# Optimization experiments

Hardware: AMD Instinct MI355X
Metric: run time of the kernel (lower is better)

## Reference

```python
import jax, jax.numpy as jnp
import numpy as np

B, N, E, H, D, MS, FF = 4, 500, 128, 8, 16, 16, 512
SQRT_D = 4.0  # sqrt_qkv_dim
EPS = 1e-5


def setup_inputs() -> dict:
    key = jax.random.key(0)
    ks = jax.random.split(key, 26)
    u = lambda k, sh, s: jax.random.uniform(k, sh, jnp.float32, -s, s)
    inp = {
        "x_edges_values": jax.random.uniform(ks[0], (B, N, N), jnp.float32),
        "depot_node_demand": jax.random.uniform(ks[1], (B, N, 1), jnp.float32),
        "rand": jax.random.uniform(ks[2], (B, E), jnp.float32),
        # attention projections (no bias)
        "Wq": u(ks[3], (E, H * D), E ** -0.5),
        "Wk": u(ks[4], (E, H * D), E ** -0.5),
        "Wv": u(ks[5], (E, H * D), E ** -0.5),
        # mixed-score per-head MLP
        "mix1_w": u(ks[6], (H, 2, MS), 0.7071067811865476),
        "mix1_b": u(ks[7], (H, MS), 0.7071067811865476),
        "mix2_w": u(ks[8], (H, MS, 1), 0.25),
        "mix2_b": u(ks[9], (H, 1), 0.25),
        # multi_head_combine
        "Wo": u(ks[10], (H * D, E), (H * D) ** -0.5),
        "bo": u(ks[11], (E,), (H * D) ** -0.5),
        # feed-forward
        "W1": u(ks[12], (E, FF), E ** -0.5),
        "b1": u(ks[13], (FF,), E ** -0.5),
        "W2": u(ks[14], (FF, E), FF ** -0.5),
        "b2": u(ks[15], (E,), FF ** -0.5),
        # batch norms (affine)
        "bn1_g": jnp.ones((E,), jnp.float32),
        "bn1_b": jnp.zeros((E,), jnp.float32),
        "bn2_g": jnp.ones((E,), jnp.float32),
        "bn2_b": jnp.zeros((E,), jnp.float32),
        # demand / node embeddings
        "Wd": u(ks[16], (1, E), 1.0),
        "bd": u(ks[17], (E,), 1.0),
        "Wn": u(ks[18], (2 * E, E), (2 * E) ** -0.5),
        "bn_node": u(ks[19], (E,), (2 * E) ** -0.5),
    }
    return inp


def _batchnorm(x, g, b):
    # BatchNorm1d in training mode over flattened [B*N, E]
    x2 = x.reshape(-1, E)
    m = x2.mean(0)
    v = ((x2 - m) ** 2).mean(0)  # biased variance, as torch uses for normalization
    return (((x2 - m) / jnp.sqrt(v + EPS)) * g + b).reshape(x.shape)


def reference(x_edges_values, depot_node_demand, rand, Wq, Wk, Wv,
              mix1_w, mix1_b, mix2_w, mix2_b, Wo, bo, W1, b1, W2, b2,
              bn1_g, bn1_b, bn2_g, bn2_b, Wd, bd, Wn, bn_node):
    # seed embeddings: row_emb zeros, col_emb scattered one-hot from a random perm
    row_emb = jnp.zeros((B, N, E), jnp.float32)
    perm = jnp.argsort(rand, axis=1)                       # [B, E] (seed_cnt = E since N > E)
    idx = jnp.concatenate([perm, perm, perm, perm], 1)[:, :N]  # 3E <= N < 4E branch
    col_emb = jax.nn.one_hot(idx, E, dtype=jnp.float32)    # [B, N, E]

    heads = lambda x: x.reshape(B, N, H, D).transpose(0, 2, 1, 3)  # [B,H,N,D]
    q = heads(row_emb @ Wq)
    k = heads(col_emb @ Wk)
    v = heads(col_emb @ Wv)

    dot = jnp.einsum('bhnd,bhmd->bhnm', q, k) / SQRT_D        # [B,H,N,N]
    cost = jnp.broadcast_to(x_edges_values[:, None], (B, H, N, N))
    two = jnp.stack([dot, cost], axis=-1)                      # [B,H,N,N,2]
    ms1 = jax.nn.relu(jnp.einsum('bhnmt,hts->bhnms', two, mix1_w)
                      + mix1_b[None, :, None, None, :])        # [B,H,N,N,MS]
    ms2 = jnp.einsum('bhnms,hso->bhnmo', ms1, mix2_w)[..., 0] \
          + mix2_b[None, :, None, :]                           # [B,H,N,N]
    weights = jax.nn.softmax(ms2, axis=-1)
    out = jnp.einsum('bhnm,bhmd->bhnd', weights, v)
    out_concat = out.transpose(0, 2, 1, 3).reshape(B, N, H * D)

    multi_head_out = out_concat @ Wo + bo
    out1 = _batchnorm(row_emb + multi_head_out, bn1_g, bn1_b)
    ff = jax.nn.relu(out1 @ W1 + b1) @ W2 + b2
    out3 = _batchnorm(out1 + ff, bn2_g, bn2_b)

    demand_feature = depot_node_demand @ Wd + bd               # [B,N,E]
    node_feature = jnp.concatenate([out3, demand_feature], -1) @ Wn + bn_node
    return node_feature
```

## Files before the change

kernel.cpp:

```cpp
#include <hip/hip_runtime.h>
#include <hip/hip_bf16.h>


#define BN_EPS 1e-5f
#define WS_X1    256000
#define WS_X2    512000
#define WS_SUM1  768000
#define WS_SQ1   768128
#define WS_SUM2  768256
#define WS_SQ2   768384
#define WS_UV    768512
#define WS_C0V   768640
#define BN1P     770000
#define BN2P     900000

#define GB8_R2(WPTR, LDW, KIDX, ACT2D, ACC)                             \
  {                                                                     \
    float4 w[8];                                                        \
    _Pragma("unroll")                                                   \
    for (int u = 0; u < 8; ++u)                                         \
      w[u] = *(const float4*)((WPTR) + (size_t)((KIDX) + u) * (LDW));   \
    _Pragma("unroll")                                                   \
    for (int u = 0; u < 8; ++u) {                                       \
      _Pragma("unroll")                                                 \
      for (int r = 0; r < 2; ++r) {                                     \
        float a = ACT2D[r][u];                                          \
        ACC[r][0] = fmaf(a, w[u].x, ACC[r][0]);                         \
        ACC[r][1] = fmaf(a, w[u].y, ACC[r][1]);                         \
        ACC[r][2] = fmaf(a, w[u].z, ACC[r][2]);                         \
        ACC[r][3] = fmaf(a, w[u].w, ACC[r][3]);                         \
      }                                                                 \
    }                                                                   \
  }

#define LD_AV2(SRC_ROW0, SRC_ROW1, KIDX, ACT2D)                         \
  {                                                                     \
    float4 x0 = *(const float4*)&(SRC_ROW0)[(KIDX)];                    \
    float4 y0 = *(const float4*)&(SRC_ROW0)[(KIDX) + 4];                \
    float4 x1 = *(const float4*)&(SRC_ROW1)[(KIDX)];                    \
    float4 y1 = *(const float4*)&(SRC_ROW1)[(KIDX) + 4];                \
    ACT2D[0][0]=x0.x; ACT2D[0][1]=x0.y; ACT2D[0][2]=x0.z; ACT2D[0][3]=x0.w; \
    ACT2D[0][4]=y0.x; ACT2D[0][5]=y0.y; ACT2D[0][6]=y0.z; ACT2D[0][7]=y0.w; \
    ACT2D[1][0]=x1.x; ACT2D[1][1]=x1.y; ACT2D[1][2]=x1.z; ACT2D[1][3]=x1.w; \
    ACT2D[1][4]=y1.x; ACT2D[1][5]=y1.y; ACT2D[1][6]=y1.z; ACT2D[1][7]=y1.w; \
  }

#define GB4_R4(WPTR, LDW, K0, SRC2D, ACC)                               \
  {                                                                     \
    float4 w[4];                                                        \
    _Pragma("unroll")                                                   \
    for (int u = 0; u < 4; ++u)                                         \
      w[u] = *(const float4*)((WPTR) + (size_t)((K0) + u) * (LDW));     \
    float av[4][4];                                                     \
    _Pragma("unroll")                                                   \
    for (int r = 0; r < 4; ++r) {                                       \
      float4 x = *(const float4*)&SRC2D[r][(K0)];                       \
      av[r][0] = x.x; av[r][1] = x.y; av[r][2] = x.z; av[r][3] = x.w;   \
    }                                                                   \
    _Pragma("unroll")                                                   \
    for (int u = 0; u < 4; ++u) {                                       \
      _Pragma("unroll")                                                 \
      for (int r = 0; r < 4; ++r) {                                     \
        ACC[r][0] = fmaf(av[r][u], w[u].x, ACC[r][0]);                  \
        ACC[r][1] = fmaf(av[r][u], w[u].y, ACC[r][1]);                  \
        ACC[r][2] = fmaf(av[r][u], w[u].z, ACC[r][2]);                  \
        ACC[r][3] = fmaf(av[r][u], w[u].w, ACC[r][3]);                  \
      }                                                                 \
    }                                                                   \
  }

__global__ __launch_bounds__(512, 4) void k_attn(const float* __restrict__ cost,
                                                 const float* __restrict__ rnd,
                                                 const float* __restrict__ Wv,
                                                 const float* __restrict__ mix1w,
                                                 const float* __restrict__ mix1b,
                                                 const float* __restrict__ mix2w,
                                                 const float* __restrict__ mix2b,
                                                 const float* __restrict__ Wo,
                                                 const float* __restrict__ bo,
                                                 float* __restrict__ ws) {
  __shared__ float scost[4][512];
  __shared__ float lutT[8 * 256];
  __shared__ float lutD[8 * 256];
  __shared__ float aw[32][132];
  __shared__ float soc[4][132];
  __shared__ float sP[8][512];
  __shared__ float svr[128];
  __shared__ int   sperm[128];
  __shared__ float mu[8][16], mr[8][16], mA[8], mB[8];
  __shared__ float sS[512], sQ[512];
  const int t = threadIdx.x;
  const int lane = t & 63;
  const int blk = blockIdx.x;
  const int row0 = blk * 4;
  const int b = blk / 125;

  {
    int rr = t >> 7, i4 = t & 127;
    *(float4*)&scost[rr][i4 * 4] = (i4 < 125)
        ? *(const float4*)(cost + (size_t)(row0 + rr) * 500 + i4 * 4)
        : float4{0.f, 0.f, 0.f, 0.f};
  }
  if (t < 128) svr[t] = rnd[b * 128 + t];
  __syncthreads();
  if (t < 128) {
    float vt = svr[t];
    int rank = 0;
    for (int j = 0; j < 128; ++j) {
      float vj = svr[j];
      rank += (vj < vt) || (vj == vt && j < t);
    }
    sperm[rank] = t;
    int h = t >> 4, s = t & 15;
    float w1  = mix1w[h * 32 + 16 + s];
    float b1v = mix1b[h * 16 + s];
    float w2  = mix2w[h * 16 + s];
    bool tiny = fabsf(w1) < 1e-20f;
    float us = tiny ? 0.f : 0.5f * w2 * fabsf(w1);
    float rs = tiny ? 0.f : -b1v / w1;
    float Ap = 0.5f * w2 * w1;
    float Bp = 0.5f * w2 * b1v + (tiny ? 0.5f * w2 * fabsf(b1v) : 0.f);
    mu[h][s] = us; mr[h][s] = rs;
#pragma unroll
    for (int off = 1; off < 16; off <<= 1) {
      Ap += __shfl_xor(Ap, off);
      Bp += __shfl_xor(Bp, off);
    }
    if (s == 0) { mA[h] = Ap; mB[h] = Bp + mix2b[h]; }
  }
  __syncthreads();
  float* traw = &sP[0][0];
  if (t < 257) {
    float x = (float)t * (1.f / 255.f);
    for (int h = 0; h < 8; ++h) {
      float g = fmaf(x, mA[h], mB[h]);
#pragma unroll
      for (int s = 0; s < 16; ++s)
        g = fmaf(fabsf(x - mr[h][s]), mu[h][s], g);
      traw[h * 257 + t] = __expf(g);
    }
  }
  __syncthreads();
#pragma unroll
  for (int p = 0; p < 4; ++p) {
    int e = t + p * 512;
    int h = e >> 8, i = e & 255;
    float a = traw[h * 257 + i];
    lutT[e] = a;
    lutD[e] = traw[h * 257 + i + 1] - a;
  }
  __syncthreads();
  {
    const int wid = t >> 6;
    const int r  = wid & 3;
    const int h0 = (wid >> 2) * 4;
    float cv8[8];
#pragma unroll
    for (int ii = 0; ii < 8; ++ii) cv8[ii] = scost[r][ii * 64 + lane];
    for (int h = h0; h < h0 + 4; ++h) {
      const float* lT = &lutT[h * 256];
      const float* lD = &lutD[h * 256];
      float wsum = 0.f, a0 = 0.f, a1 = 0.f;
#pragma unroll
      for (int ii = 0; ii < 8; ++ii) {
        float u = cv8[ii] * 255.f;
        int i = (int)u;
        float f = u - (float)i;
        float e = fmaf(lD[i], f, lT[i]);
        if (ii == 7 && lane >= 52) e = 0.f;
        wsum += e;
        if (ii & 1) a1 += e; else a0 += e;
      }
#pragma unroll
      for (int off = 32; off; off >>= 1) wsum += __shfl_xor(wsum, off);
      float inv = 1.f / wsum;
      aw[r * 8 + h][lane]      = a0 * inv;
      aw[r * 8 + h][64 + lane] = a1 * inv;
    }
  }
  __syncthreads();
  {
    const int c  = t & 127;
    const int jh = t >> 7;
    const int h  = c >> 4;
    float acc4[4] = {0.f, 0.f, 0.f, 0.f};
    for (int jb = jh * 32; jb < jh * 32 + 32; jb += 8) {
      int rows[8];
#pragma unroll
      for (int u = 0; u < 8; ++u) rows[u] = sperm[jb + u];
      float wv8[8];
#pragma unroll
      for (int u = 0; u < 8; ++u) wv8[u] = Wv[(size_t)rows[u] * 128 + c];
#pragma unroll
      for (int r = 0; r < 4; ++r) {
        float4 aa = *(const float4*)&aw[r * 8 + h][jb];
        float4 ab = *(const float4*)&aw[r * 8 + h][jb + 4];
        acc4[r] = fmaf(aa.x, wv8[0], acc4[r]);
        acc4[r] = fmaf(aa.y, wv8[1], acc4[r]);
        acc4[r] = fmaf(aa.z, wv8[2], acc4[r]);
        acc4[r] = fmaf(aa.w, wv8[3], acc4[r]);
        acc4[r] = fmaf(ab.x, wv8[4], acc4[r]);
        acc4[r] = fmaf(ab.y, wv8[5], acc4[r]);
        acc4[r] = fmaf(ab.z, wv8[6], acc4[r]);
        acc4[r] = fmaf(ab.w, wv8[7], acc4[r]);
      }
    }
#pragma unroll
    for (int r = 0; r < 4; ++r) sP[jh][r * 128 + c] = acc4[r];
  }
  __syncthreads();
  {
    int r = t >> 7, c = t & 127;
    soc[r][c] = sP[0][r * 128 + c] + sP[1][r * 128 + c] +
                sP[2][r * 128 + c] + sP[3][r * 128 + c];
  }
  __syncthreads();
  {
    const int cg  = (t & 31) * 4;
    const int seg = (t >> 5) & 7;
    const int rh  = t >> 8;
    const int k0  = seg * 16;
    float acc[2][4] = {};
    float av[2][8];
#pragma unroll
    for (int kb = 0; kb < 16; kb += 8) {
      LD_AV2(soc[rh * 2], soc[rh * 2 + 1], k0 + kb, av);
      GB8_R2(Wo + cg, 128, k0 + kb, av, acc);
    }
#pragma unroll
    for (int r = 0; r < 2; ++r)
      *(float4*)&sP[seg][(rh * 2 + r) * 128 + cg] = *(float4*)acc[r];
  }
  __syncthreads();
  {
    int r = t >> 7, col = t & 127;
    float x = bo[col];
#pragma unroll
    for (int sg = 0; sg < 8; ++sg) x += sP[sg][r * 128 + col];
    ws[WS_X1 + (size_t)(row0 + r) * 128 + col] = x;
    sS[t] = x; sQ[t] = x * x;
  }
  __syncthreads();
  if (t < 128) {
    ws[BN1P + blk * 256 + t]       = sS[t] + sS[t+128] + sS[t+256] + sS[t+384];
    ws[BN1P + blk * 256 + 128 + t] = sQ[t] + sQ[t+128] + sQ[t+256] + sQ[t+384];
  }
}

__global__ __launch_bounds__(256) void k_red(const float* __restrict__ Wn,
                                             const float* __restrict__ Wd,
                                             const float* __restrict__ bd,
                                             const float* __restrict__ bnn,
                                             float* __restrict__ ws,
                                             int src, int nslots, int dst) {
  const int t = threadIdx.x;
  if (blockIdx.x < 32) {
    __shared__ float red[32][9];
    const int col = blockIdx.x * 8 + (t & 7);
    const int strip = t >> 3;
    float s = 0.f;
    for (int j = strip; j < nslots; j += 32) s += ws[src + j * 256 + col];
    red[strip][t & 7] = s;
    __syncthreads();
    if (t < 8) {
      float x = 0.f;
#pragma unroll
      for (int k = 0; k < 32; ++k) x += red[k][t];
      ws[dst + blockIdx.x * 8 + t] = x;
    }
  } else {
    __shared__ float ru[2][128], rc[2][128];
    const int c = t & 127, g = t >> 7;
    float u = 0.f, cc = 0.f;
#pragma unroll 8
    for (int e = g * 64; e < g * 64 + 64; ++e) {
      float wn = Wn[(size_t)(128 + e) * 128 + c];
      u  = fmaf(Wd[e], wn, u);
      cc = fmaf(bd[e], wn, cc);
    }
    ru[g][c] = u; rc[g][c] = cc;
    __syncthreads();
    if (t < 128) {
      ws[WS_UV + t]  = ru[0][t] + ru[1][t];
      ws[WS_C0V + t] = rc[0][t] + rc[1][t] + bnn[t];
    }
  }
}

__global__ __launch_bounds__(512, 2) void k_ffn(const float* __restrict__ W1,
                                                const float* __restrict__ b1,
                                                const float* __restrict__ g1,
                                                const float* __restrict__ bb1,
                                                const float* __restrict__ W2,
                                                const float* __restrict__ b2,
                                                float* __restrict__ ws) {
  __shared__ float o1[4][128];
  __shared__ float sY[4][512];
  __shared__ float sP[4][4][512];
  __shared__ float sS[512], sQ[512];
  const int t = threadIdx.x;
  const int blk = blockIdx.x;
  const int row0 = blk * 4;
  const int c0 = t & 127;
  float m1 = ws[WS_SUM1 + c0] * 5e-4f;
  float v1 = ws[WS_SQ1 + c0] * 5e-4f - m1 * m1;
  float scv = g1[c0] * rsqrtf(v1 + BN_EPS);
  float shv = bb1[c0] - m1 * scv;
  {
    int r = t >> 7;
    o1[r][c0] = ws[WS_X1 + (size_t)(row0 + r) * 128 + c0] * scv + shv;
  }
  __syncthreads();
  {
    const int cg   = (t & 127) * 4;
    const int kseg = t >> 7;
    const int kb0  = kseg * 32;
    float acc[4][4] = {};
#pragma unroll
    for (int kb = 0; kb < 32; kb += 4)
      GB4_R4(W1 + cg, 512, kb0 + kb, o1, acc);
#pragma unroll
    for (int r = 0; r < 4; ++r)
      *(float4*)&sP[kseg][r][cg] = *(float4*)acc[r];
  }
  __syncthreads();
#pragma unroll
  for (int i = 0; i < 4; ++i) {
    int idx = t + i * 512;
    int r = idx >> 9, c = idx & 511;
    float x = sP[0][r][c] + sP[1][r][c] + sP[2][r][c] + sP[3][r][c];
    sY[r][c] = fmaxf(x + b1[c], 0.f);
  }
  __syncthreads();
  float* p2 = &sP[0][0][0];
  {
    const int cg   = (t & 31) * 4;
    const int kseg = t >> 5;
    const int kb0  = kseg * 32;
    float acc[4][4] = {};
#pragma unroll
    for (int kb = 0; kb < 32; kb += 4)
      GB4_R4(W2 + cg, 128, kb0 + kb, sY, acc);
#pragma unroll
    for (int r = 0; r < 4; ++r)
      *(float4*)(p2 + (size_t)(kseg * 4 + r) * 128 + cg) = *(float4*)acc[r];
  }
  __syncthreads();
  {
    int r = t >> 7, c = t & 127;
    float x = b2[c] + o1[r][c];
#pragma unroll
    for (int sg = 0; sg < 16; ++sg) x += p2[(size_t)(sg * 4 + r) * 128 + c];
    ws[WS_X2 + (size_t)(row0 + r) * 128 + c] = x;
    sS[t] = x; sQ[t] = x * x;
  }
  __syncthreads();
  if (t < 128) {
    ws[BN2P + blk * 256 + t]       = sS[t] + sS[t+128] + sS[t+256] + sS[t+384];
    ws[BN2P + blk * 256 + 128 + t] = sQ[t] + sQ[t+128] + sQ[t+256] + sQ[t+384];
  }
}

__global__ __launch_bounds__(512, 4) void k_final(const float* __restrict__ Wn,
                                                  const float* __restrict__ g2,
                                                  const float* __restrict__ bb2,
                                                  const float* __restrict__ dem,
                                                  float* __restrict__ outp,
                                                  float* __restrict__ ws) {
  __shared__ float o3[4][132];
  __shared__ float sP[8][4][128];
  const int t = threadIdx.x;
  const int blk = blockIdx.x;
  const int row0 = blk * 4;
  const int c0 = t & 127;
  float m2 = ws[WS_SUM2 + c0] * 5e-4f;
  float v2 = ws[WS_SQ2 + c0] * 5e-4f - m2 * m2;
  float scv = g2[c0] * rsqrtf(v2 + BN_EPS);
  float shv = bb2[c0] - m2 * scv;
  {
    int r = t >> 7;
    o3[r][c0] = ws[WS_X2 + (size_t)(row0 + r) * 128 + c0] * scv + shv;
  }
  __syncthreads();
  {
    const int cg  = (t & 31) * 4;
    const int seg = (t >> 5) & 7;
    const int rh  = t >> 8;
    const int k0  = seg * 16;
    float acc[2][4] = {};
    float av[2][8];
#pragma unroll
    for (int kb = 0; kb < 16; kb += 8) {
      LD_AV2(o3[rh * 2], o3[rh * 2 + 1], k0 + kb, av);
      GB8_R2(Wn + cg, 128, k0 + kb, av, acc);
    }
#pragma unroll
    for (int r = 0; r < 2; ++r)
      *(float4*)&sP[seg][rh * 2 + r][cg] = *(float4*)acc[r];
  }
  __syncthreads();
  {
    int r = t >> 7;
    float x = ws[WS_C0V + c0] + dem[row0 + r] * ws[WS_UV + c0];
#pragma unroll
    for (int sg = 0; sg < 8; ++sg) x += sP[sg][r][c0];
    outp[(size_t)(row0 + r) * 128 + c0] = x;
  }
}

extern "C" void kernel_launch(void* const* d_in, const int* in_sizes, int n_in,
                              void* d_out, int out_size, void* d_ws, size_t ws_size,
                              hipStream_t stream) {
  const float* cost   = (const float*)d_in[0];
  const float* dem    = (const float*)d_in[1];
  const float* rnd    = (const float*)d_in[2];
  const float* Wv     = (const float*)d_in[5];
  const float* mix1w  = (const float*)d_in[6];
  const float* mix1b  = (const float*)d_in[7];
  const float* mix2w  = (const float*)d_in[8];
  const float* mix2b  = (const float*)d_in[9];
  const float* Wo     = (const float*)d_in[10];
  const float* bo     = (const float*)d_in[11];
  const float* W1     = (const float*)d_in[12];
  const float* b1     = (const float*)d_in[13];
  const float* W2     = (const float*)d_in[14];
  const float* b2     = (const float*)d_in[15];
  const float* g1     = (const float*)d_in[16];
  const float* bb1    = (const float*)d_in[17];
  const float* g2     = (const float*)d_in[18];
  const float* bb2    = (const float*)d_in[19];
  const float* Wd     = (const float*)d_in[20];
  const float* bd     = (const float*)d_in[21];
  const float* Wn     = (const float*)d_in[22];
  const float* bnn    = (const float*)d_in[23];
  float* ws  = (float*)d_ws;
  float* out = (float*)d_out;

  hipLaunchKernelGGL(k_attn,  dim3(500), dim3(512), 0, stream, cost, rnd, Wv,
                     mix1w, mix1b, mix2w, mix2b, Wo, bo, ws);
  hipLaunchKernelGGL(k_red,   dim3(33),  dim3(256), 0, stream, Wn, Wd, bd, bnn,
                     ws, BN1P, 500, WS_SUM1);
  hipLaunchKernelGGL(k_ffn,   dim3(500), dim3(512), 0, stream, W1, b1, g1, bb1,
                     W2, b2, ws);
  hipLaunchKernelGGL(k_red,   dim3(32),  dim3(256), 0, stream, Wn, Wd, bd, bnn,
                     ws, BN2P, 500, WS_SUM2);
  hipLaunchKernelGGL(k_final, dim3(500), dim3(512), 0, stream, Wn, g2, bb2, dem,
                     out, ws);
}
```

Measured before the change: 49.23 us.

## Fuse five kernel launches into one cooperative persistent kernel with grid syncs

Replaces the five sequential launches (attention, BN1 reduction, FFN, BN2 reduction, final projection) with a single cooperative kernel of 250 blocks. Each block processes two row-tiles per phase, and grid.sync separates the phases. The goal is to remove per-launch overhead and inter-kernel gaps. It also interleaves the LUT tables into float2 so one LDS read fetches both values, and widens the reduction blocks. The cost is grid-wide barrier latency, fewer blocks (250 vs 500) with lower occupancy bounds, and a union shared-memory footprint. If the cooperative launch fails, it falls back to separate kernels.

```diff
diff --git a/kernel.cpp b/kernel.cpp
--- a/kernel.cpp
+++ b/kernel.cpp
@@ -1,5 +1,8 @@
 #include <hip/hip_runtime.h>
 #include <hip/hip_bf16.h>
+#include <hip/hip_cooperative_groups.h>
+
+namespace cg = cooperative_groups;
 
 
 #define BN_EPS 1e-5f
@@ -13,6 +16,12 @@
 #define WS_C0V   768640
 #define BN1P     770000
 #define BN2P     900000
+
+struct P {
+  const float *cost, *rnd, *dem, *Wv, *mix1w, *mix1b, *mix2w, *mix2b, *Wo, *bo;
+  const float *W1, *b1, *g1, *bb1, *W2, *b2, *Wn, *Wd, *bd, *bnn, *g2, *bb2;
+  float *out, *ws;
+};
 
 #define GB8_R2(WPTR, LDW, KIDX, ACT2D, ACC)                             \
   {                                                                     \
@@ -69,85 +78,88 @@
     }                                                                   \
   }
 
-__global__ __launch_bounds__(512, 4) void k_attn(const float* __restrict__ cost,
-                                                 const float* __restrict__ rnd,
-                                                 const float* __restrict__ Wv,
-                                                 const float* __restrict__ mix1w,
-                                                 const float* __restrict__ mix1b,
-                                                 const float* __restrict__ mix2w,
-                                                 const float* __restrict__ mix2b,
-                                                 const float* __restrict__ Wo,
-                                                 const float* __restrict__ bo,
-                                                 float* __restrict__ ws) {
-  __shared__ float scost[4][512];
-  __shared__ float lutT[8 * 256];
-  __shared__ float lutD[8 * 256];
-  __shared__ float aw[32][132];
-  __shared__ float soc[4][132];
-  __shared__ float sP[8][512];
-  __shared__ float svr[128];
-  __shared__ int   sperm[128];
-  __shared__ float mu[8][16], mr[8][16], mA[8], mB[8];
-  __shared__ float sS[512], sQ[512];
+struct SmA {
+  float scost[4][512];
+  float2 lut[2048];
+  float aw[32][132];
+  float soc[4][132];
+  float sP[8][512];
+  float svr[128];
+  float mu[8][16], mr[8][16], mA[8], mB[8];
+  int   sperm[128];
+  float sS[512], sQ[512];
+};
+struct SmF {
+  float o1[4][128];
+  float sY[4][512];
+  float sP[4][4][512];
+  float sS[512], sQ[512];
+};
+struct SmC {
+  float o3[4][132];
+  float sP[8][4][128];
+};
+struct SmR { float stage[512]; };
+union Sm { SmA a; SmF f; SmC c; SmR r; };
+
+__device__ __forceinline__ void attn_phase(const P& p, int blk, SmA& a) {
   const int t = threadIdx.x;
   const int lane = t & 63;
-  const int blk = blockIdx.x;
   const int row0 = blk * 4;
   const int b = blk / 125;
-
+  float* ws = p.ws;
   {
     int rr = t >> 7, i4 = t & 127;
-    *(float4*)&scost[rr][i4 * 4] = (i4 < 125)
-        ? *(const float4*)(cost + (size_t)(row0 + rr) * 500 + i4 * 4)
+    *(float4*)&a.scost[rr][i4 * 4] = (i4 < 125)
+        ? *(const float4*)(p.cost + (size_t)(row0 + rr) * 500 + i4 * 4)
         : float4{0.f, 0.f, 0.f, 0.f};
   }
-  if (t < 128) svr[t] = rnd[b * 128 + t];
+  if (t < 128) a.svr[t] = p.rnd[b * 128 + t];
   __syncthreads();
   if (t < 128) {
-    float vt = svr[t];
+    float vt = a.svr[t];
     int rank = 0;
     for (int j = 0; j < 128; ++j) {
-      float vj = svr[j];
+      float vj = a.svr[j];
       rank += (vj < vt) || (vj == vt && j < t);
     }
-    sperm[rank] = t;
+    a.sperm[rank] = t;
     int h = t >> 4, s = t & 15;
-    float w1  = mix1w[h * 32 + 16 + s];
-    float b1v = mix1b[h * 16 + s];
-    float w2  = mix2w[h * 16 + s];
+    float w1  = p.mix1w[h * 32 + 16 + s];
+    float b1v = p.mix1b[h * 16 + s];
+    float w2  = p.mix2w[h * 16 + s];
     bool tiny = fabsf(w1) < 1e-20f;
     float us = tiny ? 0.f : 0.5f * w2 * fabsf(w1);
     float rs = tiny ? 0.f : -b1v / w1;
     float Ap = 0.5f * w2 * w1;
     float Bp = 0.5f * w2 * b1v + (tiny ? 0.5f * w2 * fabsf(b1v) : 0.f);
-    mu[h][s] = us; mr[h][s] = rs;
+    a.mu[h][s] = us; a.mr[h][s] = rs;
 #pragma unroll
     for (int off = 1; off < 16; off <<= 1) {
       Ap += __shfl_xor(Ap, off);
       Bp += __shfl_xor(Bp, off);
     }
-    if (s == 0) { mA[h] = Ap; mB[h] = Bp + mix2b[h]; }
-  }
-  __syncthreads();
-  float* traw = &sP[0][0];
+    if (s == 0) { a.mA[h] = Ap; a.mB[h] = Bp + p.mix2b[h]; }
+  }
+  __syncthreads();
+  float* traw = &a.sP[0][0];
   if (t < 257) {
     float x = (float)t * (1.f / 255.f);
     for (int h = 0; h < 8; ++h) {
-      float g = fmaf(x, mA[h], mB[h]);
+      float g = fmaf(x, a.mA[h], a.mB[h]);
 #pragma unroll
       for (int s = 0; s < 16; ++s)
-        g = fmaf(fabsf(x - mr[h][s]), mu[h][s], g);
+        g = fmaf(fabsf(x - a.mr[h][s]), a.mu[h][s], g);
       traw[h * 257 + t] = __expf(g);
     }
   }
   __syncthreads();
 #pragma unroll
-  for (int p = 0; p < 4; ++p) {
-    int e = t + p * 512;
+  for (int pq = 0; pq < 4; ++pq) {
+    int e = t + pq * 512;
     int h = e >> 8, i = e & 255;
-    float a = traw[h * 257 + i];
-    lutT[e] = a;
-    lutD[e] = traw[h * 257 + i + 1] - a;
+    float av = traw[h * 257 + i];
+    a.lut[e] = float2{av, traw[h * 257 + i + 1] - av};
   }
   __syncthreads();
   {
@@ -156,17 +168,17 @@
     const int h0 = (wid >> 2) * 4;
     float cv8[8];
 #pragma unroll
-    for (int ii = 0; ii < 8; ++ii) cv8[ii] = scost[r][ii * 64 + lane];
+    for (int ii = 0; ii < 8; ++ii) cv8[ii] = a.scost[r][ii * 64 + lane];
     for (int h = h0; h < h0 + 4; ++h) {
-      const float* lT = &lutT[h * 256];
-      const float* lD = &lutD[h * 256];
+      const float2* lh = &a.lut[h * 256];
       float wsum = 0.f, a0 = 0.f, a1 = 0.f;
 #pragma unroll
       for (int ii = 0; ii < 8; ++ii) {
         float u = cv8[ii] * 255.f;
         int i = (int)u;
         float f = u - (float)i;
-        float e = fmaf(lD[i], f, lT[i]);
+        float2 td = lh[i];
+        float e = fmaf(td.y, f, td.x);
         if (ii == 7 && lane >= 52) e = 0.f;
         wsum += e;
         if (ii & 1) a1 += e; else a0 += e;
@@ -174,8 +186,8 @@
 #pragma unroll
       for (int off = 32; off; off >>= 1) wsum += __shfl_xor(wsum, off);
       float inv = 1.f / wsum;
-      aw[r * 8 + h][lane]      = a0 * inv;
-      aw[r * 8 + h][64 + lane] = a1 * inv;
+      a.aw[r * 8 + h][lane]      = a0 * inv;
+      a.aw[r * 8 + h][64 + lane] = a1 * inv;
     }
   }
   __syncthreads();
@@ -187,14 +199,14 @@
     for (int jb = jh * 32; jb < jh * 32 + 32; jb += 8) {
       int rows[8];
 #pragma unroll
-      for (int u = 0; u < 8; ++u) rows[u] = sperm[jb + u];
+      for (int u = 0; u < 8; ++u) rows[u] = a.sperm[jb + u];
       float wv8[8];
 #pragma unroll
-      for (int u = 0; u < 8; ++u) wv8[u] = Wv[(size_t)rows[u] * 128 + c];
+      for (int u = 0; u < 8; ++u) wv8[u] = p.Wv[(size_t)rows[u] * 128 + c];
 #pragma unroll
       for (int r = 0; r < 4; ++r) {
-        float4 aa = *(const float4*)&aw[r * 8 + h][jb];
-        float4 ab = *(const float4*)&aw[r * 8 + h][jb + 4];
+        float4 aa = *(const float4*)&a.aw[r * 8 + h][jb];
+        float4 ab = *(const float4*)&a.aw[r * 8 + h][jb + 4];
         acc4[r] = fmaf(aa.x, wv8[0], acc4[r]);
         acc4[r] = fmaf(aa.y, wv8[1], acc4[r]);
         acc4[r] = fmaf(aa.z, wv8[2], acc4[r]);
@@ -206,13 +218,13 @@
       }
     }
 #pragma unroll
-    for (int r = 0; r < 4; ++r) sP[jh][r * 128 + c] = acc4[r];
+    for (int r = 0; r < 4; ++r) a.sP[jh][r * 128 + c] = acc4[r];
   }
   __syncthreads();
   {
     int r = t >> 7, c = t & 127;
-    soc[r][c] = sP[0][r * 128 + c] + sP[1][r * 128 + c] +
-                sP[2][r * 128 + c] + sP[3][r * 128 + c];
+    a.soc[r][c] = a.sP[0][r * 128 + c] + a.sP[1][r * 128 + c] +
+                  a.sP[2][r * 128 + c] + a.sP[3][r * 128 + c];
   }
   __syncthreads();
   {
@@ -224,91 +236,82 @@
     float av[2][8];
 #pragma unroll
     for (int kb = 0; kb < 16; kb += 8) {
-      LD_AV2(soc[rh * 2], soc[rh * 2 + 1], k0 + kb, av);
-      GB8_R2(Wo + cg, 128, k0 + kb, av, acc);
+      LD_AV2(a.soc[rh * 2], a.soc[rh * 2 + 1], k0 + kb, av);
+      GB8_R2(p.Wo + cg, 128, k0 + kb, av, acc);
     }
 #pragma unroll
     for (int r = 0; r < 2; ++r)
-      *(float4*)&sP[seg][(rh * 2 + r) * 128 + cg] = *(float4*)acc[r];
+      *(float4*)&a.sP[seg][(rh * 2 + r) * 128 + cg] = *(float4*)acc[r];
   }
   __syncthreads();
   {
     int r = t >> 7, col = t & 127;
-    float x = bo[col];
-#pragma unroll
-    for (int sg = 0; sg < 8; ++sg) x += sP[sg][r * 128 + col];
+    float x = p.bo[col];
+#pragma unroll
+    for (int sg = 0; sg < 8; ++sg) x += a.sP[sg][r * 128 + col];
     ws[WS_X1 + (size_t)(row0 + r) * 128 + col] = x;
-    sS[t] = x; sQ[t] = x * x;
+    a.sS[t] = x; a.sQ[t] = x * x;
   }
   __syncthreads();
   if (t < 128) {
-    ws[BN1P + blk * 256 + t]       = sS[t] + sS[t+128] + sS[t+256] + sS[t+384];
-    ws[BN1P + blk * 256 + 128 + t] = sQ[t] + sQ[t+128] + sQ[t+256] + sQ[t+384];
-  }
-}
-
-__global__ __launch_bounds__(256) void k_red(const float* __restrict__ Wn,
-                                             const float* __restrict__ Wd,
-                                             const float* __restrict__ bd,
-                                             const float* __restrict__ bnn,
-                                             float* __restrict__ ws,
-                                             int src, int nslots, int dst) {
+    ws[BN1P + blk * 256 + t] =
+        a.sS[t] + a.sS[t+128] + a.sS[t+256] + a.sS[t+384];
+    ws[BN1P + blk * 256 + 128 + t] =
+        a.sQ[t] + a.sQ[t+128] + a.sQ[t+256] + a.sQ[t+384];
+  }
+}
+
+__device__ __forceinline__ void red_cols(const P& p, int blk, SmR& r,
+                                         int src, int dst) {
   const int t = threadIdx.x;
-  if (blockIdx.x < 32) {
-    __shared__ float red[32][9];
-    const int col = blockIdx.x * 8 + (t & 7);
-    const int strip = t >> 3;
-    float s = 0.f;
-    for (int j = strip; j < nslots; j += 32) s += ws[src + j * 256 + col];
-    red[strip][t & 7] = s;
-    __syncthreads();
-    if (t < 8) {
-      float x = 0.f;
-#pragma unroll
-      for (int k = 0; k < 32; ++k) x += red[k][t];
-      ws[dst + blockIdx.x * 8 + t] = x;
-    }
-  } else {
-    __shared__ float ru[2][128], rc[2][128];
-    const int c = t & 127, g = t >> 7;
-    float u = 0.f, cc = 0.f;
+  const int col = blk * 8 + (t & 7);
+  const int strip = t >> 3;
+  float s = 0.f;
+  for (int j = strip; j < 500; j += 64) s += p.ws[src + j * 256 + col];
+  r.stage[t] = s;
+  __syncthreads();
+  if (t < 8) {
+    float x = 0.f;
+#pragma unroll
+    for (int k = 0; k < 64; ++k) x += r.stage[k * 8 + t];
+    p.ws[dst + blk * 8 + t] = x;
+  }
+}
+
+__device__ __forceinline__ void uc0_phase(const P& p, SmR& r) {
+  const int t = threadIdx.x;
+  const int c = t & 127, g = t >> 7;
+  float u = 0.f, cc = 0.f;
 #pragma unroll 8
-    for (int e = g * 64; e < g * 64 + 64; ++e) {
-      float wn = Wn[(size_t)(128 + e) * 128 + c];
-      u  = fmaf(Wd[e], wn, u);
-      cc = fmaf(bd[e], wn, cc);
-    }
-    ru[g][c] = u; rc[g][c] = cc;
-    __syncthreads();
-    if (t < 128) {
-      ws[WS_UV + t]  = ru[0][t] + ru[1][t];
-      ws[WS_C0V + t] = rc[0][t] + rc[1][t] + bnn[t];
-    }
-  }
-}
-
-__global__ __launch_bounds__(512, 2) void k_ffn(const float* __restrict__ W1,
-                                                const float* __restrict__ b1,
-                                                const float* __restrict__ g1,
-                                                const float* __restrict__ bb1,
-                                                const float* __restrict__ W2,
-                                                const float* __restrict__ b2,
-                                                float* __restrict__ ws) {
-  __shared__ float o1[4][128];
-  __shared__ float sY[4][512];
-  __shared__ float sP[4][4][512];
-  __shared__ float sS[512], sQ[512];
+  for (int e = g * 32; e < g * 32 + 32; ++e) {
+    float wn = p.Wn[(size_t)(128 + e) * 128 + c];
+    u  = fmaf(p.Wd[e], wn, u);
+    cc = fmaf(p.bd[e], wn, cc);
+  }
+  r.stage[t] = u;
+  __syncthreads();
+  if (t < 128)
+    p.ws[WS_UV + t] = r.stage[t] + r.stage[t+128] + r.stage[t+256] + r.stage[t+384];
+  __syncthreads();
+  r.stage[t] = cc;
+  __syncthreads();
+  if (t < 128)
+    p.ws[WS_C0V + t] = r.stage[t] + r.stage[t+128] + r.stage[t+256] +
+                       r.stage[t+384] + p.bnn[t];
+}
+
+__device__ __forceinline__ void ffn_phase(const P& p, int blk, SmF& f) {
   const int t = threadIdx.x;
-  const int blk = blockIdx.x;
   const int row0 = blk * 4;
+  float* ws = p.ws;
   const int c0 = t & 127;
   float m1 = ws[WS_SUM1 + c0] * 5e-4f;
   float v1 = ws[WS_SQ1 + c0] * 5e-4f - m1 * m1;
-  float scv = g1[c0] * rsqrtf(v1 + BN_EPS);
-  float shv = bb1[c0] - m1 * scv;
+  float scv = p.g1[c0] * rsqrtf(v1 + BN_EPS);
+  float shv = p.bb1[c0] - m1 * scv;
   {
     int r = t >> 7;
-    o1[r][c0] = ws[WS_X1 + (size_t)(row0 + r) * 128 + c0] * scv + shv;
+    f.o1[r][c0] = ws[WS_X1 + (size_t)(row0 + r) * 128 + c0] * scv + shv;
   }
   __syncthreads();
   {
@@ -318,21 +321,21 @@
     float acc[4][4] = {};
 #pragma unroll
     for (int kb = 0; kb < 32; kb += 4)
-      GB4_R4(W1 + cg, 512, kb0 + kb, o1, acc);
+      GB4_R4(p.W1 + cg, 512, kb0 + kb, f.o1, acc);
 #pragma unroll
     for (int r = 0; r < 4; ++r)
-      *(float4*)&sP[kseg][r][cg] = *(float4*)acc[r];
+      *(float4*)&f.sP[kseg][r][cg] = *(float4*)acc[r];
   }
   __syncthreads();
 #pragma unroll
   for (int i = 0; i < 4; ++i) {
     int idx = t + i * 512;
     int r = idx >> 9, c = idx & 511;
-    float x = sP[0][r][c] + sP[1][r][c] + sP[2][r][c] + sP[3][r][c];
-    sY[r][c] = fmaxf(x + b1[c], 0.f);
-  }
-  __syncthreads();
-  float* p2 = &sP[0][0][0];
+    float x = f.sP[0][r][c] + f.sP[1][r][c] + f.sP[2][r][c] + f.sP[3][r][c];
+    f.sY[r][c] = fmaxf(x + p.b1[c], 0.f);
+  }
+  __syncthreads();
+  float* p2 = &f.sP[0][0][0];
   {
     const int cg   = (t & 31) * 4;
     const int kseg = t >> 5;
@@ -340,7 +343,7 @@
     float acc[4][4] = {};
 #pragma unroll
     for (int kb = 0; kb < 32; kb += 4)
-      GB4_R4(W2 + cg, 128, kb0 + kb, sY, acc);
+      GB4_R4(p.W2 + cg, 128, kb0 + kb, f.sY, acc);
 #pragma unroll
     for (int r = 0; r < 4; ++r)
       *(float4*)(p2 + (size_t)(kseg * 4 + r) * 128 + cg) = *(float4*)acc[r];
@@ -348,38 +351,33 @@
   __syncthreads();
   {
     int r = t >> 7, c = t & 127;
-    float x = b2[c] + o1[r][c];
+    float x = p.b2[c] + f.o1[r][c];
 #pragma unroll
     for (int sg = 0; sg < 16; ++sg) x += p2[(size_t)(sg * 4 + r) * 128 + c];
     ws[WS_X2 + (size_t)(row0 + r) * 128 + c] = x;
-    sS[t] = x; sQ[t] = x * x;
+    f.sS[t] = x; f.sQ[t] = x * x;
   }
   __syncthreads();
   if (t < 128) {
-    ws[BN2P + blk * 256 + t]       = sS[t] + sS[t+128] + sS[t+256] + sS[t+384];
-    ws[BN2P + blk * 256 + 128 + t] = sQ[t] + sQ[t+128] + sQ[t+256] + sQ[t+384];
-  }
-}
-
-__global__ __launch_bounds__(512, 4) void k_final(const float* __restrict__ Wn,
-                                                  const float* __restrict__ g2,
-                                                  const float* __restrict__ bb2,
-                                                  const float* __restrict__ dem,
-                                                  float* __restrict__ outp,
-                                                  float* __restrict__ ws) {
-  __shared__ float o3[4][132];
-  __shared__ float sP[8][4][128];
+    ws[BN2P + blk * 256 + t] =
+        f.sS[t] + f.sS[t+128] + f.sS[t+256] + f.sS[t+384];
+    ws[BN2P + blk * 256 + 128 + t] =
+        f.sQ[t] + f.sQ[t+128] + f.sQ[t+256] + f.sQ[t+384];
+  }
+}
+
+__device__ __forceinline__ void final_phase(const P& p, int blk, SmC& c) {
   const int t = threadIdx.x;
-  const int blk = blockIdx.x;
   const int row0 = blk * 4;
+  float* ws = p.ws;
   const int c0 = t & 127;
   float m2 = ws[WS_SUM2 + c0] * 5e-4f;
   float v2 = ws[WS_SQ2 + c0] * 5e-4f - m2 * m2;
-  float scv = g2[c0] * rsqrtf(v2 + BN_EPS);
-  float shv = bb2[c0] - m2 * scv;
+  float scv = p.g2[c0] * rsqrtf(v2 + BN_EPS);
+  float shv = p.bb2[c0] - m2 * scv;
   {
     int r = t >> 7;
-    o3[r][c0] = ws[WS_X2 + (size_t)(row0 + r) * 128 + c0] * scv + shv;
+    c.o3[r][c0] = ws[WS_X2 + (size_t)(row0 + r) * 128 + c0] * scv + shv;
   }
   __syncthreads();
   {
@@ -391,59 +389,105 @@
     float av[2][8];
 #pragma unroll
     for (int kb = 0; kb < 16; kb += 8) {
-      LD_AV2(o3[rh * 2], o3[rh * 2 + 1], k0 + kb, av);
-      GB8_R2(Wn + cg, 128, k0 + kb, av, acc);
+      LD_AV2(c.o3[rh * 2], c.o3[rh * 2 + 1], k0 + kb, av);
+      GB8_R2(p.Wn + cg, 128, k0 + kb, av, acc);
     }
 #pragma unroll
     for (int r = 0; r < 2; ++r)
-      *(float4*)&sP[seg][rh * 2 + r][cg] = *(float4*)acc[r];
+      *(float4*)&c.sP[seg][rh * 2 + r][cg] = *(float4*)acc[r];
   }
   __syncthreads();
   {
     int r = t >> 7;
-    float x = ws[WS_C0V + c0] + dem[row0 + r] * ws[WS_UV + c0];
-#pragma unroll
-    for (int sg = 0; sg < 8; ++sg) x += sP[sg][r][c0];
-    outp[(size_t)(row0 + r) * 128 + c0] = x;
-  }
+    float x = ws[WS_C0V + c0] + p.dem[row0 + r] * ws[WS_UV + c0];
+#pragma unroll
+    for (int sg = 0; sg < 8; ++sg) x += c.sP[sg][r][c0];
+    p.out[(size_t)(row0 + r) * 128 + c0] = x;
+  }
+}
+
+__global__ __launch_bounds__(512, 2) void k_mega(P p) {
+  cg::grid_group grid = cg::this_grid();
+  __shared__ Sm sm;
+  const int bid = blockIdx.x;
+  attn_phase(p, bid, sm.a);
+  __syncthreads();
+  attn_phase(p, bid + 250, sm.a);
+  grid.sync();
+  if (bid < 32) red_cols(p, bid, sm.r, BN1P, WS_SUM1);
+  else if (bid == 32) uc0_phase(p, sm.r);
+  grid.sync();
+  ffn_phase(p, bid, sm.f);
+  __syncthreads();
+  ffn_phase(p, bid + 250, sm.f);
+  grid.sync();
+  if (bid < 32) red_cols(p, bid, sm.r, BN2P, WS_SUM2);
+  grid.sync();
+  final_phase(p, bid, sm.c);
+  __syncthreads();
+  final_phase(p, bid + 250, sm.c);
+}
+
+__global__ __launch_bounds__(512, 4) void k_attn_s(P p) {
+  __shared__ SmA a;
+  attn_phase(p, blockIdx.x, a);
+}
+__global__ __launch_bounds__(512) void k_red1_s(P p) {
+  __shared__ SmR r;
+  if (blockIdx.x < 32) red_cols(p, blockIdx.x, r, BN1P, WS_SUM1);
+  else uc0_phase(p, r);
+}
+__global__ __launch_bounds__(512, 2) void k_ffn_s(P p) {
+  __shared__ SmF f;
+  ffn_phase(p, blockIdx.x, f);
+}
+__global__ __launch_bounds__(512) void k_red2_s(P p) {
+  __shared__ SmR r;
+  red_cols(p, blockIdx.x, r, BN2P, WS_SUM2);
+}
+__global__ __launch_bounds__(512, 4) void k_final_s(P p) {
+  __shared__ SmC c;
+  final_phase(p, blockIdx.x, c);
 }
 
 extern "C" void kernel_launch(void* const* d_in, const int* in_sizes, int n_in,
                               void* d_out, int out_size, void* d_ws, size_t ws_size,
                               hipStream_t stream) {
-  const float* cost   = (const float*)d_in[0];
-  const float* dem    = (const float*)d_in[1];
-  const float* rnd    = (const float*)d_in[2];
-  const float* Wv     = (const float*)d_in[5];
-  const float* mix1w  = (const float*)d_in[6];
-  const float* mix1b  = (const float*)d_in[7];
-  const float* mix2w  = (const float*)d_in[8];
-  const float* mix2b  = (const float*)d_in[9];
-  const float* Wo     = (const float*)d_in[10];
-  const float* bo     = (const float*)d_in[11];
-  const float* W1     = (const float*)d_in[12];
-  const float* b1     = (const float*)d_in[13];
-  const float* W2     = (const float*)d_in[14];
-  const float* b2     = (const float*)d_in[15];
-  const float* g1     = (const float*)d_in[16];
-  const float* bb1    = (const float*)d_in[17];
-  const float* g2     = (const float*)d_in[18];
-  const float* bb2    = (const float*)d_in[19];
-  const float* Wd     = (const float*)d_in[20];
-  const float* bd     = (const float*)d_in[21];
-  const float* Wn     = (const float*)d_in[22];
-  const float* bnn    = (const float*)d_in[23];
-  float* ws  = (float*)d_ws;
-  float* out = (float*)d_out;
-
-  hipLaunchKernelGGL(k_attn,  dim3(500), dim3(512), 0, stream, cost, rnd, Wv,
-                     mix1w, mix1b, mix2w, mix2b, Wo, bo, ws);
-  hipLaunchKernelGGL(k_red,   dim3(33),  dim3(256), 0, stream, Wn, Wd, bd, bnn,
-                     ws, BN1P, 500, WS_SUM1);
-  hipLaunchKernelGGL(k_ffn,   dim3(500), dim3(512), 0, stream, W1, b1, g1, bb1,
-                     W2, b2, ws);
-  hipLaunchKernelGGL(k_red,   dim3(32),  dim3(256), 0, stream, Wn, Wd, bd, bnn,
-                     ws, BN2P, 500, WS_SUM2);
-  hipLaunchKernelGGL(k_final, dim3(500), dim3(512), 0, stream, Wn, g2, bb2, dem,
-                     out, ws);
-}
+  P p;
+  p.cost  = (const float*)d_in[0];
+  p.dem   = (const float*)d_in[1];
+  p.rnd   = (const float*)d_in[2];
+  p.Wv    = (const float*)d_in[5];
+  p.mix1w = (const float*)d_in[6];
+  p.mix1b = (const float*)d_in[7];
+  p.mix2w = (const float*)d_in[8];
+  p.mix2b = (const float*)d_in[9];
+  p.Wo    = (const float*)d_in[10];
+  p.bo    = (const float*)d_in[11];
+  p.W1    = (const float*)d_in[12];
+  p.b1    = (const float*)d_in[13];
+  p.W2    = (const float*)d_in[14];
+  p.b2    = (const float*)d_in[15];
+  p.g1    = (const float*)d_in[16];
+  p.bb1   = (const float*)d_in[17];
+  p.g2    = (const float*)d_in[18];
+  p.bb2   = (const float*)d_in[19];
+  p.Wd    = (const float*)d_in[20];
+  p.bd    = (const float*)d_in[21];
+  p.Wn    = (const float*)d_in[22];
+  p.bnn   = (const float*)d_in[23];
+  p.out   = (float*)d_out;
+  p.ws    = (float*)d_ws;
+
+  void* args[] = { (void*)&p };
+  hipError_t rc = hipLaunchCooperativeKernel((const void*)k_mega, dim3(250),
+                                             dim3(512), args, 0, stream);
+  if (rc != hipSuccess) {
+    (void)hipGetLastError();
+    hipLaunchKernelGGL(k_attn_s,  dim3(500), dim3(512), 0, stream, p);
+    hipLaunchKernelGGL(k_red1_s,  dim3(33),  dim3(512), 0, stream, p);
+    hipLaunchKernelGGL(k_ffn_s,   dim3(500), dim3(512), 0, stream, p);
+    hipLaunchKernelGGL(k_red2_s,  dim3(32),  dim3(512), 0, stream, p);
+    hipLaunchKernelGGL(k_final_s, dim3(500), dim3(512), 0, stream, p);
+  }
+}
```

Result: slower. 177.8 us (+261.1%).
